# Optimization experiments

Measured on AMD Instinct MI355X. Metric: run time of the kernel, lower is better.

Reference implementation:

```python
import jax, jax.numpy as jnp
import numpy as np

N_NODES = 50000
N_EDGES = 625000
HIDDEN = 128
N_GRAPHS = 256
N_CLASSES = 10


def setup_inputs() -> dict:
    key = jax.random.key(0)
    ks = jax.random.split(key, 8)
    x = jax.random.normal(ks[0], (N_NODES, 1), dtype=jnp.float32)
    edge_index = jax.random.randint(ks[1], (2, N_EDGES), 0, N_NODES, dtype=jnp.int32)
    # balanced, sorted graph assignment -> every graph segment non-empty
    batch_index = (jnp.arange(N_NODES, dtype=jnp.int32) * N_GRAPHS) // N_NODES
    s = 1.0 / np.sqrt(HIDDEN)
    W1 = jax.random.normal(ks[2], (1, HIDDEN), dtype=jnp.float32)
    b1 = jnp.zeros((HIDDEN,), dtype=jnp.float32)
    W2 = jax.random.normal(ks[3], (HIDDEN, HIDDEN), dtype=jnp.float32) * s
    b2 = jnp.zeros((HIDDEN,), dtype=jnp.float32)
    Wout = jax.random.normal(ks[4], (2 * HIDDEN, N_CLASSES), dtype=jnp.float32) * (1.0 / np.sqrt(2 * HIDDEN))
    bout = jnp.zeros((N_CLASSES,), dtype=jnp.float32)
    return {"x": x, "edge_index": edge_index, "batch_index": batch_index,
            "W1": W1, "b1": b1, "W2": W2, "b2": b2, "Wout": Wout, "bout": bout}


def _gcn_norm(edge_index, n_nodes):
    # add self loops, compute symmetric normalization coefficients (PyG GCNConv)
    loop = jnp.arange(n_nodes, dtype=edge_index.dtype)
    src = jnp.concatenate([edge_index[0], loop])
    dst = jnp.concatenate([edge_index[1], loop])
    deg = jax.ops.segment_sum(jnp.ones_like(dst, dtype=jnp.float32), dst,
                              num_segments=n_nodes)
    dis = jnp.where(deg > 0, jax.lax.rsqrt(jnp.maximum(deg, 1.0)), 0.0)
    norm = dis[src] * dis[dst]  # [E + N]
    return src, dst, norm


def _gcn_conv(x, W, b, src, dst, norm, n_nodes):
    h = x @ W                                   # [N, out]
    msgs = h[src] * norm[:, None]               # [E+N, out] gather + scale
    agg = jax.ops.segment_sum(msgs, dst, num_segments=n_nodes)  # scatter-add
    return agg + b


def reference(x, edge_index, batch_index, W1, b1, W2, b2, Wout, bout):
    n = x.shape[0]
    src, dst, norm = _gcn_norm(edge_index, n)
    h = jax.nn.relu(_gcn_conv(x, W1, b1, src, dst, norm, n))
    # dropout p=0.5 with training=False -> identity
    h = jax.nn.relu(_gcn_conv(h, W2, b2, src, dst, norm, n))
    gmax = jax.ops.segment_max(h, batch_index, num_segments=N_GRAPHS)
    gsum = jax.ops.segment_sum(h, batch_index, num_segments=N_GRAPHS)
    cnt = jax.ops.segment_sum(jnp.ones((n,), dtype=h.dtype), batch_index,
                              num_segments=N_GRAPHS)
    gmean = gsum / jnp.maximum(cnt, 1.0)[:, None]
    pooled = jnp.concatenate([gmax, gmean], axis=1)  # [G, 2*hidden]
    logits = pooled @ Wout + bout
    return jax.nn.softmax(logits, axis=1)
```

## Files before the change

### kernel.cpp

```cpp
#include <hip/hip_runtime.h>
#include <math.h>
#include <float.h>

#define H 128
#define NCLS 10
#define CAP 64
#define NSB 512
#define BINSZ 256
#define NBINS 196
#define CAPPB 24

__global__ void pa_bin(const int* __restrict__ ei, int E, int N,
                       int* __restrict__ binbuf, int* __restrict__ cntmat) {
  __shared__ int scnt[BINSZ];
  __shared__ int sbuf[NBINS * CAPPB];
  int t = threadIdx.x;
  int blk = blockIdx.x;
  scnt[t] = 0;
  __syncthreads();
  int ePer = (E + NSB - 1) / NSB;
  int e0 = blk * ePer, e1 = min(E, e0 + ePer);
  for (int e = e0 + t; e < e1; e += 256) {
    int src = ei[e];
    int dst = ei[E + e];
    int bin = dst >> 8;
    int dstl = dst & 255;
    int pos = atomicAdd(&scnt[bin], 1);
    if (pos < CAPPB) sbuf[bin * CAPPB + pos] = (dstl << 16) | src;
  }
  __syncthreads();
  if (t < NBINS) cntmat[blk * 256 + t] = min(scnt[t], CAPPB);
  int* dstb = &binbuf[blk * (NBINS * CAPPB)];
  for (int i = t; i < NBINS * CAPPB; i += 256) dstb[i] = sbuf[i];
}

__global__ void pb_fill_tables(const int* __restrict__ binbuf, const int* __restrict__ cntmat,
                               int N, int G,
                               const float* __restrict__ x, const int* __restrict__ batch,
                               int* __restrict__ cnt, int* __restrict__ csr,
                               float* __restrict__ dis, float* __restrict__ ux,
                               int* __restrict__ gstart,
                               const float* __restrict__ W1, const float* __restrict__ b1,
                               const float* __restrict__ W2,
                               float* __restrict__ sortedt, float4* __restrict__ tab4) {
  int t = threadIdx.x;
  if ((int)blockIdx.x < NBINS) {
    __shared__ int cnt_l[BINSZ];
    int b = blockIdx.x;
    int lo = b * BINSZ;
    int nNodes = min(N - lo, BINSZ);
    cnt_l[t] = 0;
    __syncthreads();
    for (int sb = t; sb < NSB; sb += 256) {
      int c = cntmat[sb * 256 + b];
      const int* seg = &binbuf[sb * (NBINS * CAPPB) + b * CAPPB];
      for (int j = 0; j < c; ++j) {
        int v = seg[j];
        int dstl = v >> 16;
        int pos = atomicAdd(&cnt_l[dstl], 1);
        if (pos < CAP) csr[(size_t)(lo + dstl) * CAP + pos] = v & 0xFFFF;
      }
    }
    __syncthreads();
    if (t < nNodes) {
      int idx = lo + t;
      int deg = cnt_l[t];
      cnt[idx] = deg;
      float d = rsqrtf((float)(deg + 1));
      dis[idx] = d;
      ux[idx] = d * x[idx];
      int bi = batch[idx];
      if (idx == 0) { gstart[0] = 0; gstart[G] = N; }
      else if (batch[idx - 1] != bi) gstart[bi] = idx;
    }
  } else {
    __shared__ float tw[H], tb[H], tt[H];
    __shared__ int tr[H];
    int s = blockIdx.x - NBINS;
    if (t < H) {
      float w = W1[t], bb = b1[t];
      tw[t] = w; tb[t] = bb;
      tt[t] = (w != 0.0f) ? (-bb / w) : INFINITY;
    }
    __syncthreads();
    if (t < H) {
      float tj = tt[t];
      int r = 0;
      for (int i = 0; i < H; ++i) {
        float ti = tt[i];
        r += (ti < tj || (ti == tj && i < t)) ? 1 : 0;
      }
      tr[t] = r;
      if (s == 0) sortedt[r] = tj;
    }
    __syncthreads();
    if (t < H) {
      float A = 0.f, B = 0.f;
      #pragma unroll 16
      for (int j = 0; j < H; ++j) {
        float wj = tw[j];
        bool act = (wj > 0.f && tr[j] < s) || (wj < 0.f && tr[j] >= s) ||
                   (wj == 0.f && tb[j] > 0.f);
        float w2 = W2[j * H + t];
        if (act) { A = fmaf(wj, w2, A); B = fmaf(tb[j], w2, B); }
      }
      float* base4 = (float*)&tab4[s * 64 + (t >> 1)];
      base4[t & 1] = A;
      base4[2 + (t & 1)] = B;
    }
  }
}

__global__ void kf_vaseg(const int* __restrict__ cnt, const int* __restrict__ csr,
                         const float* __restrict__ ux, const float* __restrict__ dis,
                         const float* __restrict__ sortedt,
                         float4* __restrict__ vaseg, int N) {
  __shared__ float t_s[H];
  if (threadIdx.x < H) t_s[threadIdx.x] = sortedt[threadIdx.x];
  __syncthreads();
  int idx = blockIdx.x * 256 + threadIdx.x;
  if (idx >= N) return;
  int len = min(cnt[idx], CAP);
  const int* row = &csr[(size_t)idx * CAP];
  float s = ux[idx];
  int j = 0;
  for (; j + 4 <= len; j += 4) {
    int4 c4 = *(const int4*)&row[j];
    float u0 = ux[c4.x], u1 = ux[c4.y], u2 = ux[c4.z], u3 = ux[c4.w];
    s += (u0 + u1) + (u2 + u3);
  }
  for (; j < len; ++j) s += ux[row[j]];
  float d = dis[idx];
  float a = d * s;
  int lo = 0, hi = H;
  while (lo < hi) { int mid = (lo + hi) >> 1; if (t_s[mid] < a) lo = mid + 1; else hi = mid; }
  vaseg[idx] = make_float4(d * a, d, __int_as_float(lo), 0.f);
}

__global__ __launch_bounds__(1024)
void kg_agg(const int* __restrict__ cnt, const int* __restrict__ csr,
            const float4* __restrict__ vaseg, const float4* __restrict__ tab4,
            const float* __restrict__ b2, const int* __restrict__ gstart,
            float* __restrict__ pmax, float* __restrict__ psum) {
  __shared__ float4 stash[16][64];
  __shared__ float lmx[16 * H];
  __shared__ float lsm[16 * H];
  int g = blockIdx.x >> 1, half = blockIdx.x & 1;
  int gs = gstart[g], ge = gstart[g + 1];
  int mid = gs + ((ge - gs) >> 1);
  int s0 = half ? mid : gs;
  int s1e = half ? ge : mid;
  int wave = threadIdx.x >> 6;
  int lane = threadIdx.x & 63;
  int k0 = lane * 2;
  float2 b2v = *(const float2*)&b2[k0];
  float mxa = -FLT_MAX, mxb = -FLT_MAX, sma = 0.f, smb = 0.f;
  for (int d = s0 + wave; d < s1e; d += 16) {
    int len = min(cnt[d], CAP);
    float4 pd = vaseg[d];
    float accx = 0.f, accy = 0.f;
    if (lane < len) {
      int sN = csr[(size_t)d * CAP + lane];
      stash[wave][lane] = vaseg[sN];
    }
    __builtin_amdgcn_wave_barrier();
    __threadfence_block();
    int sg0 = __float_as_int(pd.z), sg1 = -1, sg2 = -1, sg3 = -1;
    float P0 = pd.x, Q0 = pd.y;
    float P1 = 0.f, Q1 = 0.f, P2 = 0.f, Q2 = 0.f, P3 = 0.f, Q3 = 0.f;
    for (int j = 0; j < len; ++j) {
      float4 ps = stash[wave][j];
      int sg = __float_as_int(ps.z);
      if (sg == sg0)      { P0 += ps.x; Q0 += ps.y; }
      else if (sg == sg1) { P1 += ps.x; Q1 += ps.y; }
      else if (sg == sg2) { P2 += ps.x; Q2 += ps.y; }
      else if (sg == sg3) { P3 += ps.x; Q3 += ps.y; }
      else if (sg1 < 0)   { sg1 = sg; P1 = ps.x; Q1 = ps.y; }
      else if (sg2 < 0)   { sg2 = sg; P2 = ps.x; Q2 = ps.y; }
      else if (sg3 < 0)   { sg3 = sg; P3 = ps.x; Q3 = ps.y; }
      else {
        float4 T = tab4[sg3 * 64 + lane];
        accx = fmaf(P3, T.x, fmaf(Q3, T.z, accx));
        accy = fmaf(P3, T.y, fmaf(Q3, T.w, accy));
        sg3 = sg; P3 = ps.x; Q3 = ps.y;
      }
    }
    __builtin_amdgcn_wave_barrier();
    {
      float4 T = tab4[sg0 * 64 + lane];
      accx = fmaf(P0, T.x, fmaf(Q0, T.z, accx));
      accy = fmaf(P0, T.y, fmaf(Q0, T.w, accy));
    }
    if (sg1 >= 0) {
      float4 T = tab4[sg1 * 64 + lane];
      accx = fmaf(P1, T.x, fmaf(Q1, T.z, accx));
      accy = fmaf(P1, T.y, fmaf(Q1, T.w, accy));
    }
    if (sg2 >= 0) {
      float4 T = tab4[sg2 * 64 + lane];
      accx = fmaf(P2, T.x, fmaf(Q2, T.z, accx));
      accy = fmaf(P2, T.y, fmaf(Q2, T.w, accy));
    }
    if (sg3 >= 0) {
      float4 T = tab4[sg3 * 64 + lane];
      accx = fmaf(P3, T.x, fmaf(Q3, T.z, accx));
      accy = fmaf(P3, T.y, fmaf(Q3, T.w, accy));
    }
    float dd = pd.y;
    float ha = fmaxf(fmaf(dd, accx, b2v.x), 0.f);
    float hb = fmaxf(fmaf(dd, accy, b2v.y), 0.f);
    mxa = fmaxf(mxa, ha); mxb = fmaxf(mxb, hb);
    sma += ha; smb += hb;
  }
  lmx[wave * H + k0] = mxa; lmx[wave * H + k0 + 1] = mxb;
  lsm[wave * H + k0] = sma; lsm[wave * H + k0 + 1] = smb;
  __syncthreads();
  int t = threadIdx.x;
  if (t < H) {
    float m = -FLT_MAX, sm = 0.f;
    #pragma unroll
    for (int w = 0; w < 16; ++w) { m = fmaxf(m, lmx[w * H + t]); sm += lsm[w * H + t]; }
    pmax[(size_t)blockIdx.x * H + t] = m;
    psum[(size_t)blockIdx.x * H + t] = sm;
  }
}

__global__ void kh_final(const float* __restrict__ pmax, const float* __restrict__ psum,
                         const int* __restrict__ gstart,
                         const float* __restrict__ Wout, const float* __restrict__ bout,
                         float* __restrict__ out) {
  int g = blockIdx.x;
  int t = threadIdx.x;
  __shared__ float pooled[2 * H];
  __shared__ float logits[NCLS];
  if (t < H) {
    float m = fmaxf(pmax[(size_t)(2 * g) * H + t], pmax[(size_t)(2 * g + 1) * H + t]);
    float sm = psum[(size_t)(2 * g) * H + t] + psum[(size_t)(2 * g + 1) * H + t];
    float cnt = (float)(gstart[g + 1] - gstart[g]);
    pooled[t] = m;
    pooled[H + t] = sm / fmaxf(cnt, 1.0f);
  }
  __syncthreads();
  if (t < NCLS) {
    float acc = bout[t];
    for (int j = 0; j < 2 * H; ++j) acc = fmaf(pooled[j], Wout[j * NCLS + t], acc);
    logits[t] = acc;
  }
  __syncthreads();
  if (t == 0) {
    float m = logits[0];
    for (int c = 1; c < NCLS; ++c) m = fmaxf(m, logits[c]);
    float ssum = 0.f;
    float ex[NCLS];
    for (int c = 0; c < NCLS; ++c) { ex[c] = expf(logits[c] - m); ssum += ex[c]; }
    float inv = 1.0f / ssum;
    for (int c = 0; c < NCLS; ++c) out[g * NCLS + c] = ex[c] * inv;
  }
}

extern "C" void kernel_launch(void* const* d_in, const int* in_sizes, int n_in,
                              void* d_out, int out_size, void* d_ws, size_t ws_size,
                              hipStream_t stream) {
  const float* x    = (const float*)d_in[0];
  const int*   ei   = (const int*)d_in[1];
  const int*   batch= (const int*)d_in[2];
  const float* W1   = (const float*)d_in[3];
  const float* b1   = (const float*)d_in[4];
  const float* W2   = (const float*)d_in[5];
  const float* b2   = (const float*)d_in[6];
  const float* Wout = (const float*)d_in[7];
  const float* bout = (const float*)d_in[8];
  float* out = (float*)d_out;

  int N = in_sizes[0];
  int E = in_sizes[1] / 2;
  int G = out_size / NCLS;

  char* ws = (char*)d_ws;
  size_t off = 0;
  auto alloc = [&](size_t bytes) {
    char* p = ws + off;
    off += (bytes + 255) & ~(size_t)255;
    return p;
  };
  int*    cnt     = (int*)alloc(sizeof(int) * N);
  int*    csr     = (int*)alloc(sizeof(int) * (size_t)N * CAP);
  int*    binbuf  = (int*)alloc(sizeof(int) * (size_t)NSB * NBINS * CAPPB);
  int*    cntmat  = (int*)alloc(sizeof(int) * NSB * 256);
  float*  dis     = (float*)alloc(sizeof(float) * N);
  float*  ux      = (float*)alloc(sizeof(float) * N);
  float*  sortedt = (float*)alloc(sizeof(float) * H);
  float4* tab4    = (float4*)alloc(sizeof(float4) * (H + 1) * 64);
  int*    gstart  = (int*)alloc(sizeof(int) * (G + 1));
  float4* vaseg   = (float4*)alloc(sizeof(float4) * N);
  float*  pmax    = (float*)alloc(sizeof(float) * 2 * G * H);
  float*  psum    = (float*)alloc(sizeof(float) * 2 * G * H);
  (void)ws_size; (void)n_in;

  int nbN = (N + 255) / 256;

  pa_bin<<<NSB, 256, 0, stream>>>(ei, E, N, binbuf, cntmat);
  pb_fill_tables<<<NBINS + H + 1, 256, 0, stream>>>(binbuf, cntmat, N, G,
                                                    x, batch, cnt, csr, dis, ux, gstart,
                                                    W1, b1, W2, sortedt, tab4);
  kf_vaseg<<<nbN, 256, 0, stream>>>(cnt, csr, ux, dis, sortedt, vaseg, N);
  kg_agg<<<2 * G, 1024, 0, stream>>>(cnt, csr, vaseg, tab4, b2, gstart, pmax, psum);
  kh_final<<<G, 256, 0, stream>>>(pmax, psum, gstart, Wout, bout, out);
}
```

Before: 157.8 us.

## Embed per-bin counts in bin buffer and vectorize CSR fill loads

Each bin segment in binbuf now stores its own edge count in slot 0, so the separate count matrix and its extra strided reads go away. The per-bin capacity grows to make room for the count. pb_fill_tables now runs 512 threads, one per superblock, and loads each segment with int4 vector reads into registers before the atomic CSR insertion, instead of looping twice with scalar loads. In exchange, every block of that kernel, including the non-bin table-building blocks, now runs at double width, and the unrolled 28-element register array raises register pressure.

Measured after the change: 159.2 us. No clear change (+0.9%).

```diff
diff --git a/kernel.cpp b/kernel.cpp
--- a/kernel.cpp
+++ b/kernel.cpp
@@ -8,15 +8,15 @@
 #define NSB 512
 #define BINSZ 256
 #define NBINS 196
-#define CAPPB 24
+#define CAPPB 28
 
 __global__ void pa_bin(const int* __restrict__ ei, int E, int N,
-                       int* __restrict__ binbuf, int* __restrict__ cntmat) {
+                       int* __restrict__ binbuf) {
   __shared__ int scnt[BINSZ];
   __shared__ int sbuf[NBINS * CAPPB];
   int t = threadIdx.x;
   int blk = blockIdx.x;
-  scnt[t] = 0;
+  scnt[t] = 1;
   __syncthreads();
   int ePer = (E + NSB - 1) / NSB;
   int e0 = blk * ePer, e1 = min(E, e0 + ePer);
@@ -29,33 +29,45 @@
     if (pos < CAPPB) sbuf[bin * CAPPB + pos] = (dstl << 16) | src;
   }
   __syncthreads();
-  if (t < NBINS) cntmat[blk * 256 + t] = min(scnt[t], CAPPB);
+  if (t < NBINS) sbuf[t * CAPPB] = min(scnt[t], CAPPB) - 1;
   int* dstb = &binbuf[blk * (NBINS * CAPPB)];
   for (int i = t; i < NBINS * CAPPB; i += 256) dstb[i] = sbuf[i];
 }
 
-__global__ void pb_fill_tables(const int* __restrict__ binbuf, const int* __restrict__ cntmat,
-                               int N, int G,
-                               const float* __restrict__ x, const int* __restrict__ batch,
-                               int* __restrict__ cnt, int* __restrict__ csr,
-                               float* __restrict__ dis, float* __restrict__ ux,
-                               int* __restrict__ gstart,
-                               const float* __restrict__ W1, const float* __restrict__ b1,
-                               const float* __restrict__ W2,
-                               float* __restrict__ sortedt, float4* __restrict__ tab4) {
+__global__ __launch_bounds__(512)
+void pb_fill_tables(const int* __restrict__ binbuf, int N, int G,
+                    const float* __restrict__ x, const int* __restrict__ batch,
+                    int* __restrict__ cnt, int* __restrict__ csr,
+                    float* __restrict__ dis, float* __restrict__ ux,
+                    int* __restrict__ gstart,
+                    const float* __restrict__ W1, const float* __restrict__ b1,
+                    const float* __restrict__ W2,
+                    float* __restrict__ sortedt, float4* __restrict__ tab4) {
   int t = threadIdx.x;
   if ((int)blockIdx.x < NBINS) {
     __shared__ int cnt_l[BINSZ];
     int b = blockIdx.x;
     int lo = b * BINSZ;
     int nNodes = min(N - lo, BINSZ);
-    cnt_l[t] = 0;
+    if (t < BINSZ) cnt_l[t] = 0;
     __syncthreads();
-    for (int sb = t; sb < NSB; sb += 256) {
-      int c = cntmat[sb * 256 + b];
-      const int* seg = &binbuf[sb * (NBINS * CAPPB) + b * CAPPB];
-      for (int j = 0; j < c; ++j) {
-        int v = seg[j];
+    const int4* seg4 = (const int4*)&binbuf[t * (NBINS * CAPPB) + b * CAPPB];
+    int4 Wk[7];
+    Wk[0] = seg4[0];
+    int c = Wk[0].x;
+    #pragma unroll
+    for (int k = 1; k < 7; ++k)
+      Wk[k] = (4 * k <= c) ? seg4[k] : make_int4(0, 0, 0, 0);
+    int arr[28];
+    #pragma unroll
+    for (int k = 0; k < 7; ++k) {
+      arr[4 * k + 0] = Wk[k].x; arr[4 * k + 1] = Wk[k].y;
+      arr[4 * k + 2] = Wk[k].z; arr[4 * k + 3] = Wk[k].w;
+    }
+    #pragma unroll
+    for (int j = 0; j < CAPPB - 1; ++j) {
+      if (j < c) {
+        int v = arr[j + 1];
         int dstl = v >> 16;
         int pos = atomicAdd(&cnt_l[dstl], 1);
         if (pos < CAP) csr[(size_t)(lo + dstl) * CAP + pos] = v & 0xFFFF;
@@ -286,7 +298,6 @@
   int*    cnt     = (int*)alloc(sizeof(int) * N);
   int*    csr     = (int*)alloc(sizeof(int) * (size_t)N * CAP);
   int*    binbuf  = (int*)alloc(sizeof(int) * (size_t)NSB * NBINS * CAPPB);
-  int*    cntmat  = (int*)alloc(sizeof(int) * NSB * 256);
   float*  dis     = (float*)alloc(sizeof(float) * N);
   float*  ux      = (float*)alloc(sizeof(float) * N);
   float*  sortedt = (float*)alloc(sizeof(float) * H);
@@ -299,8 +310,8 @@
 
   int nbN = (N + 255) / 256;
 
-  pa_bin<<<NSB, 256, 0, stream>>>(ei, E, N, binbuf, cntmat);
-  pb_fill_tables<<<NBINS + H + 1, 256, 0, stream>>>(binbuf, cntmat, N, G,
+  pa_bin<<<NSB, 256, 0, stream>>>(ei, E, N, binbuf);
+  pb_fill_tables<<<NBINS + H + 1, 512, 0, stream>>>(binbuf, N, G,
                                                     x, batch, cnt, csr, dis, ux, gstart,
                                                     W1, b1, W2, sortedt, tab4);
   kf_vaseg<<<nbN, 256, 0, stream>>>(cnt, csr, ux, dis, sortedt, vaseg, N);
```
